# Performance work log

Measured on AMD Instinct MI355X. Metric: run time of the kernel, lower is better.

## Reference

```python
import jax, jax.numpy as jnp
import numpy as np

B, S, D, DFF = 8, 2048, 1024, 4096

def setup_inputs() -> dict:
    key = jax.random.key(0)
    ks = jax.random.split(key, 11)
    s = 0.02
    return {
        "x":  jax.random.normal(ks[0], (B, S, D), dtype=jnp.float32),
        "Wq": jax.random.normal(ks[1], (D, D), dtype=jnp.float32) * s,
        "bq": jnp.zeros((D,), dtype=jnp.float32),
        "Wk": jax.random.normal(ks[2], (D, D), dtype=jnp.float32) * s,
        "bk": jnp.zeros((D,), dtype=jnp.float32),
        "Wv": jax.random.normal(ks[3], (D, D), dtype=jnp.float32) * s,
        "bv": jnp.zeros((D,), dtype=jnp.float32),
        "W1": jax.random.normal(ks[4], (DFF, D), dtype=jnp.float32) * s,
        "b1": jnp.zeros((DFF,), dtype=jnp.float32),
        "W2": jax.random.normal(ks[5], (D, DFF), dtype=jnp.float32) * s,
        "b2": jnp.zeros((D,), dtype=jnp.float32),
    }

def reference(x, Wq, bq, Wk, bk, Wv, bv, W1, b1, W2, b2):
    # qkv projections (torch Linear: x @ W.T + b)
    q = jnp.einsum('bsd,ed->bse', x, Wq) + bq
    k = jnp.einsum('bsd,ed->bse', x, Wk) + bk
    v = jnp.einsum('bsd,ed->bse', x, Wv) + bv
    # single-head scaled dot-product attention with causal mask (decoder=True)
    scale = 1.0 / jnp.sqrt(jnp.asarray(q.shape[-1], q.dtype))
    scores = jnp.einsum('bqd,bkd->bqk', q, k) * scale  # (B,S,S)
    causal = jnp.tril(jnp.ones((scores.shape[-2], scores.shape[-1]), dtype=bool))
    scores = jnp.where(causal, scores, jnp.asarray(-jnp.inf, scores.dtype))
    attn = jax.nn.softmax(scores, axis=-1)
    attn_out = jnp.einsum('bqk,bkd->bqd', attn, v)
    # MLP: linear_2(gelu(linear_1(.)))  — exact (erf) GELU as in torch default
    h = jax.nn.gelu(jnp.einsum('bsd,fd->bsf', attn_out, W1) + b1, approximate=False)
    return jnp.einsum('bsf,df->bsd', h, W2) + b2
```

## Files before the change

### kernel.cpp

```cpp
#include <hip/hip_runtime.h>
#include <hip/hip_bf16.h>

#define NB   8
#define SS   2048
#define DD   1024
#define DFFN 4096
#define MTOT (NB*SS)

typedef unsigned short u16;
typedef __attribute__((ext_vector_type(4))) float f32x4;
typedef __attribute__((ext_vector_type(8))) short bf16x8;
typedef __attribute__((ext_vector_type(4))) int i32x4;
typedef __attribute__((ext_vector_type(4))) unsigned short u16x4;
typedef __attribute__((ext_vector_type(8))) unsigned short u16x8;

__device__ __forceinline__ u16 f2bf(float f) {
  union { float f; unsigned u; } c; c.f = f;
  unsigned r = c.u + 0x7FFFu + ((c.u >> 16) & 1u);
  return (u16)(r >> 16);
}

__device__ __forceinline__ void gload16(const void* g, void* l) {
  __builtin_amdgcn_global_load_lds(
      (const __attribute__((address_space(1))) void*)(unsigned long long)g,
      (__attribute__((address_space(3))) void*)(unsigned)(unsigned long long)l,
      16, 0, 0);
}

__device__ __forceinline__ bf16x8 dsr128(unsigned addr) {
  i32x4 r;
  asm volatile("ds_read_b128 %0, %1" : "=v"(r) : "v"(addr));
  return __builtin_bit_cast(bf16x8, r);
}

template<int EBIAS, int EGELU, int ESCALE, int EROWSCALE, int OUTMODE, int ETRANS, int CSKIP, int CK>
__global__ __launch_bounds__(256, 3)
void gemm128(const u16* __restrict__ A, const u16* __restrict__ B,
             const float* __restrict__ bias, const float* __restrict__ rowscale,
             void* __restrict__ C,
             int K, int lda, int ldb, int ldc, float scale,
             long long sA, long long sB, long long sC, int sRS)
{
  __shared__ __align__(1024) u16 smem[16384];

  const int nwg = gridDim.x * gridDim.y;
  const int orig = blockIdx.y * gridDim.x + blockIdx.x;
  const int q = nwg >> 3, r = nwg & 7;
  const int xcd = orig & 7, pos0 = orig >> 3;
  const int wg = (xcd < r ? xcd * (q + 1) : r * (q + 1) + (xcd - r) * q) + pos0;
  const int bx = wg % gridDim.x, by = wg / gridDim.x;
  const int row0 = by * 128, col0 = bx * 128;
  if (CSKIP && col0 > row0 + 127) return;

  const int z = blockIdx.z;
  A += (size_t)z * sA;
  B += (size_t)z * sB;

  int nkt = K >> 5;
  if (CK) { int lim = (row0 + 128) >> 5; if (lim < nkt) nkt = lim; }

  const int tid  = threadIdx.x;
  const int wid  = tid >> 6;
  const int lane = tid & 63;
  const int wr = wid >> 1, wc = wid & 1;

  const int srow = wid * 16 + (lane >> 2);
  const int sunit = (lane & 3) ^ ((lane >> 3) & 3);
  const char* gA = (const char*)A + ((size_t)(row0 + srow) * lda + sunit * 8) * 2;
  const char* gB = (const char*)B + ((size_t)(col0 + srow) * ldb + sunit * 8) * 2;
  char* lbase = (char*)smem;
  const size_t ldab = (size_t)64 * lda * 2;
  const size_t ldbb = (size_t)64 * ldb * 2;

  #define STG(t2) { char* lb = lbase + ((t2) & 1) * 16384; size_t kb = (size_t)(t2) * 64; \
      gload16(gA + kb,        lb + wid * 1024);                                           \
      gload16(gA + kb + ldab, lb + 4096 + wid * 1024);                                    \
      gload16(gB + kb,        lb + 8192 + wid * 1024);                                    \
      gload16(gB + kb + ldbb, lb + 8192 + 4096 + wid * 1024); }

  const int fr = lane & 15;
  const int ks16 = ((lane >> 4) & 3) * 16;
  const int xm = ((lane >> 1) & 3) << 4;
  const unsigned sbase = (unsigned)(unsigned long long)(void*)smem;

  f32x4 acc[4][4] = {};

  STG(0);
  asm volatile("s_waitcnt vmcnt(0)");
  asm volatile("s_barrier" ::: "memory");

  for (int t = 0; t < nkt; ++t) {
    if (t + 1 < nkt) STG(t + 1);
    const unsigned cb = sbase + (t & 1) * 16384;
    bf16x8 af[4], bf[4];
#pragma unroll
    for (int m = 0; m < 4; ++m)
      af[m] = dsr128(cb + (((wr * 64 + m * 16 + fr) * 64 + ks16) ^ xm));
#pragma unroll
    for (int n = 0; n < 4; ++n)
      bf[n] = dsr128(cb + ((8192 + (wc * 64 + n * 16 + fr) * 64 + ks16) ^ xm));
    asm volatile("s_waitcnt lgkmcnt(0)");
    __builtin_amdgcn_sched_barrier(0);
    __builtin_amdgcn_s_setprio(1);
#pragma unroll
    for (int m = 0; m < 4; ++m)
#pragma unroll
      for (int n = 0; n < 4; ++n)
        acc[m][n] = __builtin_amdgcn_mfma_f32_16x16x32_bf16(af[m], bf[n], acc[m][n], 0, 0, 0);
    __builtin_amdgcn_s_setprio(0);
    asm volatile("s_waitcnt vmcnt(0)");
    asm volatile("s_barrier" ::: "memory");
  }
  #undef STG

  char* sm = (char*)smem;
  const int r4 = (lane >> 4) * 4;

  if (OUTMODE == 1) {
#pragma unroll
    for (int p = 0; p < 2; ++p) {
      if (wc == p) {
#pragma unroll
        for (int n = 0; n < 4; ++n) {
          const int col = col0 + wc * 64 + n * 16 + fr;
          const int pb = (n * 16 + fr) * 4;
          float bia = EBIAS ? bias[col] : 0.0f;
#pragma unroll
          for (int m = 0; m < 4; ++m) {
#pragma unroll
            for (int j = 0; j < 4; ++j) {
              const int line = wr * 64 + m * 16 + r4 + j;
              float xv = acc[m][n][j];
              if (EBIAS)     xv += bia;
              if (ESCALE)    xv *= scale;
              if (EROWSCALE) xv *= rowscale[z * sRS + row0 + line];
              if (EGELU)     xv = 0.5f * xv * (1.0f + erff(xv * 0.70710678118f));
              *(float*)(sm + ((line * 256 + pb) ^ ((line & 7) << 4))) = xv;
            }
          }
        }
      }
      __syncthreads();
      float* Cb = (float*)C + (size_t)z * sC;
#pragma unroll
      for (int i = 0; i < 8; ++i) {
        const int o = i * 4096 + tid * 16;
        const int line = o >> 8, ps = o & 255;
        f32x4 v = *(const f32x4*)(sm + ((line * 256 + ps) ^ ((line & 7) << 4)));
        *(f32x4*)((char*)(Cb + (size_t)(row0 + line) * ldc + col0 + p * 64) + ps) = v;
      }
      __syncthreads();
    }
  } else if (ETRANS) {
#pragma unroll
    for (int n = 0; n < 4; ++n) {
      const int col = col0 + wc * 64 + n * 16 + fr;
      const int line = wc * 64 + n * 16 + fr;
      float bia = EBIAS ? bias[col] : 0.0f;
#pragma unroll
      for (int m = 0; m < 4; ++m) {
        const int rb = wr * 64 + m * 16 + r4;
        u16x4 pk;
#pragma unroll
        for (int j = 0; j < 4; ++j) {
          float xv = acc[m][n][j];
          if (EBIAS) xv += bia;
          pk[j] = f2bf(xv);
        }
        *(u16x4*)(sm + ((line * 256 + rb * 2) ^ ((line & 7) << 4))) = pk;
      }
    }
    __syncthreads();
    u16* Cb = (u16*)C + (size_t)(row0 >> 11) * (DD * SS) + (row0 & (SS - 1));
#pragma unroll
    for (int i = 0; i < 8; ++i) {
      const int o = i * 4096 + tid * 16;
      const int line = o >> 8, ps = o & 255;
      f32x4 v = *(const f32x4*)(sm + ((line * 256 + ps) ^ ((line & 7) << 4)));
      *(f32x4*)((char*)(Cb + (size_t)(col0 + line) * SS) + ps) = v;
    }
  } else {
#pragma unroll
    for (int n = 0; n < 4; ++n) {
      const int col = col0 + wc * 64 + n * 16 + fr;
      const int pc = (wc * 64 + n * 16 + fr) * 2;
      float bia = EBIAS ? bias[col] : 0.0f;
#pragma unroll
      for (int m = 0; m < 4; ++m) {
#pragma unroll
        for (int j = 0; j < 4; ++j) {
          const int line = wr * 64 + m * 16 + r4 + j;
          float xv = acc[m][n][j];
          if (EBIAS)     xv += bia;
          if (ESCALE)    xv *= scale;
          if (EROWSCALE) xv *= rowscale[z * sRS + row0 + line];
          if (EGELU)     xv = 0.5f * xv * (1.0f + erff(xv * 0.70710678118f));
          u16 u;
          if (OUTMODE == 2) { union { u16 s; _Float16 h; } cu; cu.h = (_Float16)xv; u = cu.s; }
          else u = f2bf(xv);
          *(u16*)(sm + ((line * 256 + pc) ^ ((line & 7) << 4))) = u;
        }
      }
    }
    __syncthreads();
    u16* Cb = (u16*)C + (size_t)z * sC + col0;
#pragma unroll
    for (int i = 0; i < 8; ++i) {
      const int o = i * 4096 + tid * 16;
      const int line = o >> 8, ps = o & 255;
      f32x4 v = *(const f32x4*)(sm + ((line * 256 + ps) ^ ((line & 7) << 4)));
      *(f32x4*)((char*)(Cb + (size_t)(row0 + line) * ldc) + ps) = v;
    }
  }
}

__global__ __launch_bounds__(256) void cvt_bf16_k(const float* __restrict__ in, u16* __restrict__ out, int n4) {
  int i = blockIdx.x * blockDim.x + threadIdx.x;
  if (i < n4) {
    float4 v = ((const float4*)in)[i];
    u16x4 o;
    o.x = f2bf(v.x); o.y = f2bf(v.y); o.z = f2bf(v.z); o.w = f2bf(v.w);
    ((u16x4*)out)[i] = o;
  }
}

__global__ __launch_bounds__(256) void softmax_k(u16* __restrict__ sc, float* __restrict__ rinv, int rows0) {
  const int widx = blockIdx.x * 4 + (threadIdx.x >> 6);
  const int lane = threadIdx.x & 63;
  u16* row = sc + (size_t)widx * SS;
  const int L = (widx & (SS - 1)) + 1;
  float mx = -1e30f;
  for (int k = 0; k < 4; ++k) {
    const int j0 = k * 512 + lane * 8;
    if (j0 < L) {
      u16x8 v = *(const u16x8*)(row + j0);
      int lim = L - j0; if (lim > 8) lim = 8;
#pragma unroll
      for (int e = 0; e < 8; ++e) {
        if (e < lim) { union { u16 u; _Float16 h; } c; c.u = v[e]; mx = fmaxf(mx, (float)c.h); }
      }
    }
  }
#pragma unroll
  for (int o = 32; o >= 1; o >>= 1) mx = fmaxf(mx, __shfl_xor(mx, o));
  float s = 0.0f;
  for (int k = 0; k < 4; ++k) {
    const int j0 = k * 512 + lane * 8;
    u16x8 v = *(const u16x8*)(row + j0);
    u16x8 w;
#pragma unroll
    for (int e = 0; e < 8; ++e) {
      const int j = j0 + e;
      float ev = 0.0f;
      if (j < L) { union { u16 u; _Float16 h; } c; c.u = v[e]; ev = __expf((float)c.h - mx); s += ev; }
      w[e] = f2bf(ev);
    }
    *(u16x8*)(row + j0) = w;
  }
#pragma unroll
  for (int o = 32; o >= 1; o >>= 1) s += __shfl_xor(s, o);
  if (lane == 0) rinv[rows0 + widx] = 1.0f / s;
}

extern "C" void kernel_launch(void* const* d_in, const int* in_sizes, int n_in,
                              void* d_out, int out_size, void* d_ws, size_t ws_size,
                              hipStream_t stream) {
  const float* x  = (const float*)d_in[0];
  const float* Wq = (const float*)d_in[1];
  const float* bq = (const float*)d_in[2];
  const float* Wk = (const float*)d_in[3];
  const float* bk = (const float*)d_in[4];
  const float* Wv = (const float*)d_in[5];
  const float* bv = (const float*)d_in[6];
  const float* W1 = (const float*)d_in[7];
  const float* b1 = (const float*)d_in[8];
  const float* W2 = (const float*)d_in[9];
  const float* b2 = (const float*)d_in[10];

  char* ws = (char*)d_ws;
  u16*  xb   = (u16*)(ws);
  u16*  Wqb  = (u16*)(ws + 33554432);
  u16*  Wkb  = (u16*)(ws + 35651584);
  u16*  Wvb  = (u16*)(ws + 37748736);
  u16*  W1b  = (u16*)(ws + 39845888);
  u16*  W2b  = (u16*)(ws + 48234496);
  u16*  Qb   = (u16*)(ws + 56623104);
  u16*  Kb   = (u16*)(ws + 90177536);
  u16*  Vtb  = (u16*)(ws + 123731968);
  float* rinv = (float*)(ws + 157286400);
  u16*  big  = (u16*)(ws + 157351936);
  u16*  att  = xb;

  const size_t base = 157351936ull;
  const size_t avail = ws_size > base ? ws_size - base : 0;
  int GB = 8; while (GB > 1 && (size_t)GB * 8388608ull > avail) GB >>= 1;
  int MC = 8192; while (MC > 2048 && (size_t)MC * 8192ull > avail) MC >>= 1;

  cvt_bf16_k<<<MTOT * DD / 4 / 256, 256, 0, stream>>>(x, xb, MTOT * DD / 4);
  cvt_bf16_k<<<DD * DD / 4 / 256, 256, 0, stream>>>(Wq, Wqb, DD * DD / 4);
  cvt_bf16_k<<<DD * DD / 4 / 256, 256, 0, stream>>>(Wk, Wkb, DD * DD / 4);
  cvt_bf16_k<<<DD * DD / 4 / 256, 256, 0, stream>>>(Wv, Wvb, DD * DD / 4);
  cvt_bf16_k<<<DFFN * DD / 4 / 256, 256, 0, stream>>>(W1, W1b, DFFN * DD / 4);
  cvt_bf16_k<<<DFFN * DD / 4 / 256, 256, 0, stream>>>(W2, W2b, DFFN * DD / 4);

  gemm128<1,0,0,0,0,0,0,0><<<dim3(DD/128, MTOT/128), 256, 0, stream>>>(
      xb, Wqb, bq, nullptr, (void*)Qb, DD, DD, DD, DD, 0.f, 0, 0, 0, 0);
  gemm128<1,0,0,0,0,0,0,0><<<dim3(DD/128, MTOT/128), 256, 0, stream>>>(
      xb, Wkb, bk, nullptr, (void*)Kb, DD, DD, DD, DD, 0.f, 0, 0, 0, 0);
  gemm128<1,0,0,0,0,1,0,0><<<dim3(DD/128, MTOT/128), 256, 0, stream>>>(
      xb, Wvb, bv, nullptr, (void*)Vtb, DD, DD, DD, DD, 0.f, 0, 0, 0, 0);

  for (int b0 = 0; b0 < NB; b0 += GB) {
    gemm128<0,0,1,0,2,0,1,0><<<dim3(SS/128, SS/128, GB), 256, 0, stream>>>(
        Qb + (size_t)b0 * SS * DD, Kb + (size_t)b0 * SS * DD, nullptr, nullptr,
        (void*)big, DD, DD, DD, SS, 0.03125f,
        (long long)SS * DD, (long long)SS * DD, (long long)SS * SS, 0);
    softmax_k<<<GB * SS / 4, 256, 0, stream>>>(big, rinv, b0 * SS);
    gemm128<0,0,0,1,0,0,0,1><<<dim3(DD/128, SS/128, GB), 256, 0, stream>>>(
        big, Vtb + (size_t)b0 * DD * SS, nullptr, rinv + (size_t)b0 * SS,
        (void*)(att + (size_t)b0 * SS * DD), SS, SS, SS, DD, 0.f,
        (long long)SS * SS, (long long)DD * SS, (long long)SS * DD, SS);
  }

  for (int c = 0; c < MTOT / MC; ++c) {
    u16* h = big;
    gemm128<1,1,0,0,0,0,0,0><<<dim3(DFFN/128, MC/128), 256, 0, stream>>>(
        att + (size_t)c * MC * DD, W1b, b1, nullptr, (void*)h,
        DD, DD, DD, DFFN, 0.f, 0, 0, 0, 0);
    gemm128<1,0,0,0,1,0,0,0><<<dim3(DD/128, MC/128), 256, 0, stream>>>(
        h, W2b, b2, nullptr, (void*)((float*)d_out + (size_t)c * MC * DD),
        DFFN, DFFN, DFFN, DD, 0.f, 0, 0, 0, 0);
  }
}
```

Before: 715.4 us.

## Fuse Q/K/V projections into one GEMM and raise occupancy and MLP chunk size

The three bf16 weight matrices are converted into one contiguous concatenated buffer, and a single GEMM launch over 3*D output columns replaces the three separate projection launches. A new output mode sends each column tile to Q, K or transposed V, choosing the matching bias and destination. Launch bounds go from 3 to 5 waves per SIMD, and the MLP chunk size cap doubles so fewer launches are needed when workspace allows. The aim is to cut launch overhead and the tail effects of small grids. Higher occupancy may force register spills, and the wider projection grid changes L2 reuse of x.

```diff
diff --git a/kernel.cpp b/kernel.cpp
--- a/kernel.cpp
+++ b/kernel.cpp
@@ -33,11 +33,12 @@
   return __builtin_bit_cast(bf16x8, r);
 }
 
-template<int EBIAS, int EGELU, int ESCALE, int EROWSCALE, int OUTMODE, int ETRANS, int CSKIP, int CK>
-__global__ __launch_bounds__(256, 3)
+template<int EBIAS, int EGELU, int ESCALE, int EROWSCALE, int OUTMODE, int CSKIP, int CK>
+__global__ __launch_bounds__(256, 5)
 void gemm128(const u16* __restrict__ A, const u16* __restrict__ B,
-             const float* __restrict__ bias, const float* __restrict__ rowscale,
-             void* __restrict__ C,
+             const float* __restrict__ bias0, const float* __restrict__ bias1,
+             const float* __restrict__ bias2, const float* __restrict__ rowscale,
+             void* __restrict__ C0, void* __restrict__ C1, void* __restrict__ C2,
              int K, int lda, int ldb, int ldc, float scale,
              long long sA, long long sB, long long sC, int sRS)
 {
@@ -68,14 +69,13 @@
   const int sunit = (lane & 3) ^ ((lane >> 3) & 3);
   const char* gA = (const char*)A + ((size_t)(row0 + srow) * lda + sunit * 8) * 2;
   const char* gB = (const char*)B + ((size_t)(col0 + srow) * ldb + sunit * 8) * 2;
-  char* lbase = (char*)smem;
   const size_t ldab = (size_t)64 * lda * 2;
   const size_t ldbb = (size_t)64 * ldb * 2;
 
-  #define STG(t2) { char* lb = lbase + ((t2) & 1) * 16384; size_t kb = (size_t)(t2) * 64; \
-      gload16(gA + kb,        lb + wid * 1024);                                           \
-      gload16(gA + kb + ldab, lb + 4096 + wid * 1024);                                    \
-      gload16(gB + kb,        lb + 8192 + wid * 1024);                                    \
+  #define STG(t2) { char* lb = (char*)smem + ((t2) & 1) * 16384; size_t kb = (size_t)(t2) * 64; \
+      gload16(gA + kb,        lb + wid * 1024);                                                 \
+      gload16(gA + kb + ldab, lb + 4096 + wid * 1024);                                          \
+      gload16(gB + kb,        lb + 8192 + wid * 1024);                                          \
       gload16(gB + kb + ldbb, lb + 8192 + 4096 + wid * 1024); }
 
   const int fr = lane & 15;
@@ -115,6 +115,10 @@
 
   char* sm = (char*)smem;
   const int r4 = (lane >> 4) * 4;
+  const int sel  = (OUTMODE == 3) ? (col0 >> 10) : 0;
+  const int oc0  = (OUTMODE == 3) ? (col0 & 1023) : col0;
+  const float* bias = (OUTMODE == 3) ? (sel == 0 ? bias0 : sel == 1 ? bias1 : bias2)
+                                     : bias0;
 
   if (OUTMODE == 1) {
 #pragma unroll
@@ -122,7 +126,7 @@
       if (wc == p) {
 #pragma unroll
         for (int n = 0; n < 4; ++n) {
-          const int col = col0 + wc * 64 + n * 16 + fr;
+          const int col = oc0 + wc * 64 + n * 16 + fr;
           const int pb = (n * 16 + fr) * 4;
           float bia = EBIAS ? bias[col] : 0.0f;
 #pragma unroll
@@ -141,48 +145,43 @@
         }
       }
       __syncthreads();
-      float* Cb = (float*)C + (size_t)z * sC;
+      float* Cb = (float*)C0 + (size_t)z * sC;
 #pragma unroll
       for (int i = 0; i < 8; ++i) {
         const int o = i * 4096 + tid * 16;
         const int line = o >> 8, ps = o & 255;
         f32x4 v = *(const f32x4*)(sm + ((line * 256 + ps) ^ ((line & 7) << 4)));
-        *(f32x4*)((char*)(Cb + (size_t)(row0 + line) * ldc + col0 + p * 64) + ps) = v;
+        *(f32x4*)((char*)(Cb + (size_t)(row0 + line) * ldc + oc0 + p * 64) + ps) = v;
       }
       __syncthreads();
     }
-  } else if (ETRANS) {
+  } else if (OUTMODE == 3 && sel == 2) {
 #pragma unroll
     for (int n = 0; n < 4; ++n) {
-      const int col = col0 + wc * 64 + n * 16 + fr;
       const int line = wc * 64 + n * 16 + fr;
-      float bia = EBIAS ? bias[col] : 0.0f;
+      float bia = EBIAS ? bias[oc0 + line] : 0.0f;
 #pragma unroll
       for (int m = 0; m < 4; ++m) {
         const int rb = wr * 64 + m * 16 + r4;
         u16x4 pk;
 #pragma unroll
-        for (int j = 0; j < 4; ++j) {
-          float xv = acc[m][n][j];
-          if (EBIAS) xv += bia;
-          pk[j] = f2bf(xv);
-        }
+        for (int j = 0; j < 4; ++j) pk[j] = f2bf(acc[m][n][j] + bia);
         *(u16x4*)(sm + ((line * 256 + rb * 2) ^ ((line & 7) << 4))) = pk;
       }
     }
     __syncthreads();
-    u16* Cb = (u16*)C + (size_t)(row0 >> 11) * (DD * SS) + (row0 & (SS - 1));
+    u16* Cb = (u16*)C2 + (size_t)(row0 >> 11) * (DD * SS) + (row0 & (SS - 1));
 #pragma unroll
     for (int i = 0; i < 8; ++i) {
       const int o = i * 4096 + tid * 16;
       const int line = o >> 8, ps = o & 255;
       f32x4 v = *(const f32x4*)(sm + ((line * 256 + ps) ^ ((line & 7) << 4)));
-      *(f32x4*)((char*)(Cb + (size_t)(col0 + line) * SS) + ps) = v;
+      *(f32x4*)((char*)(Cb + (size_t)(oc0 + line) * SS) + ps) = v;
     }
   } else {
 #pragma unroll
     for (int n = 0; n < 4; ++n) {
-      const int col = col0 + wc * 64 + n * 16 + fr;
+      const int col = oc0 + wc * 64 + n * 16 + fr;
       const int pc = (wc * 64 + n * 16 + fr) * 2;
       float bia = EBIAS ? bias[col] : 0.0f;
 #pragma unroll
@@ -203,7 +202,7 @@
       }
     }
     __syncthreads();
-    u16* Cb = (u16*)C + (size_t)z * sC + col0;
+    u16* Cb = (u16*)(OUTMODE == 3 ? (sel ? C1 : C0) : C0) + (size_t)z * sC + oc0;
 #pragma unroll
     for (int i = 0; i < 8; ++i) {
       const int o = i * 4096 + tid * 16;
@@ -279,9 +278,7 @@
 
   char* ws = (char*)d_ws;
   u16*  xb   = (u16*)(ws);
-  u16*  Wqb  = (u16*)(ws + 33554432);
-  u16*  Wkb  = (u16*)(ws + 35651584);
-  u16*  Wvb  = (u16*)(ws + 37748736);
+  u16*  Wcat = (u16*)(ws + 33554432);
   u16*  W1b  = (u16*)(ws + 39845888);
   u16*  W2b  = (u16*)(ws + 48234496);
   u16*  Qb   = (u16*)(ws + 56623104);
@@ -294,41 +291,43 @@
   const size_t base = 157351936ull;
   const size_t avail = ws_size > base ? ws_size - base : 0;
   int GB = 8; while (GB > 1 && (size_t)GB * 8388608ull > avail) GB >>= 1;
-  int MC = 8192; while (MC > 2048 && (size_t)MC * 8192ull > avail) MC >>= 1;
+  int MC = 16384; while (MC > 2048 && (size_t)MC * 8192ull > avail) MC >>= 1;
 
   cvt_bf16_k<<<MTOT * DD / 4 / 256, 256, 0, stream>>>(x, xb, MTOT * DD / 4);
-  cvt_bf16_k<<<DD * DD / 4 / 256, 256, 0, stream>>>(Wq, Wqb, DD * DD / 4);
-  cvt_bf16_k<<<DD * DD / 4 / 256, 256, 0, stream>>>(Wk, Wkb, DD * DD / 4);
-  cvt_bf16_k<<<DD * DD / 4 / 256, 256, 0, stream>>>(Wv, Wvb, DD * DD / 4);
+  cvt_bf16_k<<<DD * DD / 4 / 256, 256, 0, stream>>>(Wq, Wcat, DD * DD / 4);
+  cvt_bf16_k<<<DD * DD / 4 / 256, 256, 0, stream>>>(Wk, Wcat + DD * DD, DD * DD / 4);
+  cvt_bf16_k<<<DD * DD / 4 / 256, 256, 0, stream>>>(Wv, Wcat + 2 * DD * DD, DD * DD / 4);
   cvt_bf16_k<<<DFFN * DD / 4 / 256, 256, 0, stream>>>(W1, W1b, DFFN * DD / 4);
   cvt_bf16_k<<<DFFN * DD / 4 / 256, 256, 0, stream>>>(W2, W2b, DFFN * DD / 4);
 
-  gemm128<1,0,0,0,0,0,0,0><<<dim3(DD/128, MTOT/128), 256, 0, stream>>>(
-      xb, Wqb, bq, nullptr, (void*)Qb, DD, DD, DD, DD, 0.f, 0, 0, 0, 0);
-  gemm128<1,0,0,0,0,0,0,0><<<dim3(DD/128, MTOT/128), 256, 0, stream>>>(
-      xb, Wkb, bk, nullptr, (void*)Kb, DD, DD, DD, DD, 0.f, 0, 0, 0, 0);
-  gemm128<1,0,0,0,0,1,0,0><<<dim3(DD/128, MTOT/128), 256, 0, stream>>>(
-      xb, Wvb, bv, nullptr, (void*)Vtb, DD, DD, DD, DD, 0.f, 0, 0, 0, 0);
+  gemm128<1,0,0,0,3,0,0><<<dim3(3 * DD / 128, MTOT / 128), 256, 0, stream>>>(
+      xb, Wcat, bq, bk, bv, nullptr, (void*)Qb, (void*)Kb, (void*)Vtb,
+      DD, DD, DD, DD, 0.f, 0, 0, 0, 0);
 
   for (int b0 = 0; b0 < NB; b0 += GB) {
-    gemm128<0,0,1,0,2,0,1,0><<<dim3(SS/128, SS/128, GB), 256, 0, stream>>>(
-        Qb + (size_t)b0 * SS * DD, Kb + (size_t)b0 * SS * DD, nullptr, nullptr,
-        (void*)big, DD, DD, DD, SS, 0.03125f,
+    gemm128<0,0,1,0,2,1,0><<<dim3(SS/128, SS/128, GB), 256, 0, stream>>>(
+        Qb + (size_t)b0 * SS * DD, Kb + (size_t)b0 * SS * DD,
+        nullptr, nullptr, nullptr, nullptr, (void*)big, nullptr, nullptr,
+        DD, DD, DD, SS, 0.03125f,
         (long long)SS * DD, (long long)SS * DD, (long long)SS * SS, 0);
     softmax_k<<<GB * SS / 4, 256, 0, stream>>>(big, rinv, b0 * SS);
-    gemm128<0,0,0,1,0,0,0,1><<<dim3(DD/128, SS/128, GB), 256, 0, stream>>>(
-        big, Vtb + (size_t)b0 * DD * SS, nullptr, rinv + (size_t)b0 * SS,
-        (void*)(att + (size_t)b0 * SS * DD), SS, SS, SS, DD, 0.f,
+    gemm128<0,0,0,1,0,0,1><<<dim3(DD/128, SS/128, GB), 256, 0, stream>>>(
+        big, Vtb + (size_t)b0 * DD * SS,
+        nullptr, nullptr, nullptr, rinv + (size_t)b0 * SS,
+        (void*)(att + (size_t)b0 * SS * DD), nullptr, nullptr,
+        SS, SS, SS, DD, 0.f,
         (long long)SS * SS, (long long)DD * SS, (long long)SS * DD, SS);
   }
 
   for (int c = 0; c < MTOT / MC; ++c) {
     u16* h = big;
-    gemm128<1,1,0,0,0,0,0,0><<<dim3(DFFN/128, MC/128), 256, 0, stream>>>(
-        att + (size_t)c * MC * DD, W1b, b1, nullptr, (void*)h,
+    gemm128<1,1,0,0,0,0,0><<<dim3(DFFN/128, MC/128), 256, 0, stream>>>(
+        att + (size_t)c * MC * DD, W1b, b1, nullptr, nullptr, nullptr,
+        (void*)h, nullptr, nullptr,
         DD, DD, DD, DFFN, 0.f, 0, 0, 0, 0);
-    gemm128<1,0,0,0,1,0,0,0><<<dim3(DD/128, MC/128), 256, 0, stream>>>(
-        h, W2b, b2, nullptr, (void*)((float*)d_out + (size_t)c * MC * DD),
+    gemm128<1,0,0,0,1,0,0><<<dim3(DD/128, MC/128), 256, 0, stream>>>(
+        h, W2b, b2, nullptr, nullptr, nullptr,
+        (void*)((float*)d_out + (size_t)c * MC * DD), nullptr, nullptr,
         DFFN, DFFN, DFFN, DD, 0.f, 0, 0, 0, 0);
   }
 }
```

Result: slower. 2.854 ms (+298.9%).
